# Optimization experiments

Measured on AMD Instinct MI355X. Metric: run time of the kernel, lower is better.

Reference implementation:

```python
import jax, jax.numpy as jnp
import numpy as np

B, C, HD, NL, NP = 2, 256, 8, 4, 4
D = C // HD
SHAPES = np.array([[128, 128], [64, 64], [32, 32], [16, 16]], dtype=np.int64)
LV = int(SHAPES.prod(axis=1).sum())  # 21760
LQ = LV


def _bilinear(v_l, loc, Hl, Wl):
    # v_l: [B, HD, Nl, D]; loc: [B, Q, HD, P, 2] normalized to [0,1]
    # Matches torch grid_sample(bilinear, padding='zeros', align_corners=False)
    Bq, Q, _, P, _ = loc.shape
    x = loc[..., 0] * Wl - 0.5
    y = loc[..., 1] * Hl - 0.5
    x0f = jnp.floor(x)
    y0f = jnp.floor(y)
    lx, ly = x - x0f, y - y0f
    x0 = x0f.astype(jnp.int32)
    y0 = y0f.astype(jnp.int32)

    def corner(xi, yi, w):
        valid = (xi >= 0) & (xi < Wl) & (yi >= 0) & (yi < Hl)
        idx = jnp.clip(yi, 0, Hl - 1) * Wl + jnp.clip(xi, 0, Wl - 1)  # [B,Q,HD,P]
        idx = idx.transpose(0, 2, 1, 3).reshape(Bq, HD, Q * P)
        g = jnp.take_along_axis(v_l, idx[..., None], axis=2).reshape(Bq, HD, Q, P, D)
        wm = jnp.where(valid, w, 0.0).transpose(0, 2, 1, 3)[..., None]  # [B,HD,Q,P,1]
        return g * wm

    return (corner(x0, y0, (1 - lx) * (1 - ly))
            + corner(x0 + 1, y0, lx * (1 - ly))
            + corner(x0, y0 + 1, (1 - lx) * ly)
            + corner(x0 + 1, y0 + 1, lx * ly))


def _msda(query, reference_points, value, shapes, W_off, b_off, W_attn, b_attn, W_val, b_val, W_out, b_out):
    # value projection -> per-head layout [B, HD, Lv, D]
    v = (value @ W_val + b_val).reshape(B, LV, HD, D).transpose(0, 2, 1, 3)
    off = (query @ W_off + b_off).reshape(B, LQ, HD, NL, NP, 2)
    aw = jax.nn.softmax((query @ W_attn + b_attn).reshape(B, LQ, HD, NL * NP), axis=-1)
    aw = aw.reshape(B, LQ, HD, NL, NP)
    norm = jnp.asarray(shapes[:, ::-1].copy(), query.dtype)  # (W_l, H_l) per level
    # sampling locations: [B, Lq, HD, NL, NP, 2]
    loc = reference_points[:, :, None, :, None, :] + off / norm[None, None, None, :, None, :]
    out = jnp.zeros((B, HD, LQ, D), query.dtype)
    start = 0
    for l in range(NL):  # small static loop over feature levels
        Hl, Wl = int(shapes[l, 0]), int(shapes[l, 1])
        samp = _bilinear(v[:, :, start:start + Hl * Wl], loc[:, :, :, l], Hl, Wl)  # [B,HD,Q,P,D]
        out = out + jnp.einsum('bhqpd,bhqp->bhqd', samp, aw[:, :, :, l].transpose(0, 2, 1, 3))
        start += Hl * Wl
    out = out.transpose(0, 2, 1, 3).reshape(B, LQ, C)
    # output projection + residual (identity = query, dropout inactive at eval)
    return out @ W_out + b_out + query


def setup_inputs():
    key = jax.random.key(0)
    ks = jax.random.split(key, 8)
    sc = 1.0 / np.sqrt(C)
    return {
        "query": jax.random.normal(ks[0], (B, LQ, C), jnp.float32),
        "reference_points": jax.random.uniform(ks[1], (B, LQ, NL, 2), dtype=jnp.float32),
        "value": jax.random.normal(ks[2], (B, LV, C), jnp.float32),
        "spatial_shapes": SHAPES,
        "level_start_index": np.concatenate([[0], np.cumsum(SHAPES.prod(axis=1))[:-1]]).astype(np.int64),
        "W_off": jax.random.normal(ks[3], (C, HD * NL * NP * 2), jnp.float32) * 0.01,
        "b_off": jax.random.normal(ks[4], (HD * NL * NP * 2,), jnp.float32) * 0.01,
        "W_attn": jax.random.normal(ks[5], (C, HD * NL * NP), jnp.float32) * 0.02,
        "b_attn": jnp.zeros((HD * NL * NP,), jnp.float32),
        "W_val": jax.random.normal(ks[6], (C, C), jnp.float32) * sc,
        "b_val": jnp.zeros((C,), jnp.float32),
        "W_out": jax.random.normal(ks[7], (C, C), jnp.float32) * sc,
        "b_out": jnp.zeros((C,), jnp.float32),
    }


def reference(query, reference_points, value, spatial_shapes, level_start_index, W_off, b_off, W_attn, b_attn, W_val, b_val, W_out, b_out):
    shapes = np.asarray(spatial_shapes)  # static level geometry
    del level_start_index  # level offsets derived directly from shapes
    return _msda(query, reference_points, value, shapes, W_off, b_off, W_attn, b_attn, W_val, b_val, W_out, b_out)
```

## Files before the change

kernel.cpp:

```cpp
#include <hip/hip_runtime.h>

#define LQN 21760
#define LVN 21760
#define BATCH 2
#define CDIM 256
#define HDN 8
#define DDIM 32
#define PADCELLS 22736

typedef __attribute__((ext_vector_type(8))) short short8;
typedef __attribute__((ext_vector_type(4))) float f32x4;
typedef __attribute__((ext_vector_type(2))) float f32x2;

__device__ __forceinline__ unsigned short f2bf(float f) {
  union { float f; unsigned int u; } v; v.f = f;
  unsigned int r = v.u + 0x7fffu + ((v.u >> 16) & 1u);
  return (unsigned short)(r >> 16);
}
__device__ __forceinline__ float bflo(unsigned int u) {
  union { unsigned int u; float f; } v; v.u = u << 16; return v.f;
}
__device__ __forceinline__ float bfhi(unsigned int u) {
  union { unsigned int u; float f; } v; v.u = u & 0xffff0000u; return v.f;
}

__global__ __launch_bounds__(256) void zero_kernel(uint4* __restrict__ p) {
  const int i = blockIdx.x * 256 + threadIdx.x;
  p[i] = (uint4){0u, 0u, 0u, 0u};
}

__global__ __launch_bounds__(256) void prep_kernel(
    const float* __restrict__ Wval, const float* __restrict__ Woff,
    const float* __restrict__ Wattn, const float* __restrict__ Wout,
    unsigned short* __restrict__ wtval, unsigned short* __restrict__ wtoa,
    unsigned short* __restrict__ wtout) {
  int idx = blockIdx.x * 256 + threadIdx.x;
  int n = idx >> 8, k = idx & 255;
  if (idx < 65536) {
    wtval[idx] = f2bf(Wval[k * 256 + n]);
    wtout[idx] = f2bf(Wout[k * 256 + n]);
  }
  if (idx < 98304) {
    float v = (n < 256) ? Woff[k * 256 + n] : Wattn[k * 128 + (n - 256)];
    wtoa[idx] = f2bf(v);
  }
}

template <int MODE>
__global__ __launch_bounds__(256) void gemm_kernel(
    const float* __restrict__ Af32, const unsigned short* __restrict__ Abf,
    const unsigned short* __restrict__ Wt, const float* __restrict__ bias0,
    const float* __restrict__ bias1, const float* __restrict__ resid,
    unsigned short* __restrict__ out_bf, float* __restrict__ out_f32) {
  constexpr int K = 256;
  constexpr int LDSS = 56;
  __shared__ unsigned short lsA[64 * LDSS];
  __shared__ unsigned short lsB[64 * LDSS];
  const int m0 = blockIdx.x * 64;
  const int n0 = blockIdx.y * 64;
  const int t = threadIdx.x;
  const int w = t >> 6;
  const int l = t & 63;
  const int fr = l & 15;
  const int kk = (l >> 4) * 8;

  f32x4 acc[4];
#pragma unroll
  for (int c = 0; c < 4; ++c) acc[c] = (f32x4){0.f, 0.f, 0.f, 0.f};

  const int srow = t >> 2;
  const int sk = (t & 3) * 8;

  for (int kt = 0; kt < K / 32; ++kt) {
    const int k0 = kt * 32;
    if (MODE == 2) {
      *(uint4*)(lsA + srow * LDSS + sk) =
          *(const uint4*)(Abf + (size_t)(m0 + srow) * K + k0 + sk);
    } else {
      const float* ap = Af32 + (size_t)(m0 + srow) * K + k0 + sk;
      float4 f0 = *(const float4*)(ap);
      float4 f1 = *(const float4*)(ap + 4);
      uint4 pk;
      pk.x = (unsigned)f2bf(f0.x) | ((unsigned)f2bf(f0.y) << 16);
      pk.y = (unsigned)f2bf(f0.z) | ((unsigned)f2bf(f0.w) << 16);
      pk.z = (unsigned)f2bf(f1.x) | ((unsigned)f2bf(f1.y) << 16);
      pk.w = (unsigned)f2bf(f1.z) | ((unsigned)f2bf(f1.w) << 16);
      *(uint4*)(lsA + srow * LDSS + sk) = pk;
    }
    *(uint4*)(lsB + srow * LDSS + sk) =
        *(const uint4*)(Wt + (size_t)(n0 + srow) * K + k0 + sk);
    __syncthreads();
    const short8 a = *(const short8*)(lsA + (w * 16 + fr) * LDSS + kk);
#pragma unroll
    for (int c = 0; c < 4; ++c) {
      const short8 b = *(const short8*)(lsB + (c * 16 + fr) * LDSS + kk);
      acc[c] = __builtin_amdgcn_mfma_f32_16x16x32_bf16(a, b, acc[c], 0, 0, 0);
    }
    __syncthreads();
  }

  const int fq = l >> 4;
#pragma unroll
  for (int c = 0; c < 4; ++c) {
#pragma unroll
    for (int r = 0; r < 4; ++r) {
      const int row = m0 + w * 16 + fq * 4 + r;
      const int col = n0 + c * 16 + fr;
      float v = acc[c][r];
      if (MODE == 0) {
        v += bias0[col];
        const int bb = (row >= LVN) ? 1 : 0;
        const int i = row - bb * LVN;
        const int lvl = (i >= 16384) + (i >= 20480) + (i >= 21504);
        const int stl = (lvl == 0) ? 0 : (lvl == 1) ? 16384 : (lvl == 2) ? 20480 : 21504;
        const int pst = (lvl == 0) ? 0 : (lvl == 1) ? 16900 : (lvl == 2) ? 21256 : 22412;
        const int lw = 7 - lvl;
        const int Wl = 128 >> lvl;
        const int loc = i - stl;
        const int y = loc >> lw;
        const int x = loc & (Wl - 1);
        const int pidx = pst + (y + 1) * (Wl + 2) + (x + 1);
        const int hh = col >> 5, d = col & 31;
        out_bf[(((size_t)(bb * HDN + hh) * PADCELLS + pidx) << 5) + d] = f2bf(v);
      } else if (MODE == 1) {
        const float bias = (col < 256) ? bias0[col] : bias1[col - 256];
        out_bf[(size_t)row * 384 + col] = f2bf(v + bias);
      } else {
        const size_t o = (size_t)row * 256 + col;
        out_f32[o] = v + bias0[col] + resid[o];
      }
    }
  }
}

__global__ __launch_bounds__(256) void sampler_kernel(
    const unsigned short* __restrict__ vbf,
    const unsigned short* __restrict__ offattn,
    const float* __restrict__ refpts,
    unsigned short* __restrict__ msout) {
  const int lid = blockIdx.x;
  const int pair = lid & 7;
  const int k = lid >> 3;
  const int img = pair * 2 + (k & 1);
  const int qchunk = k >> 1;
  const int h = img & 7;
  const int bb = img >> 3;

  const int t = threadIdx.x;
  const int lane = t & 63;
  const int qloc = qchunk * 64 + (t >> 6) * 16 + (lane >> 2);
  const int qi = bb * LQN + qloc;
  const int d0 = (lane & 3) * 8;

  const unsigned short* oa = offattn + (size_t)qi * 384;

  float lg[16];
  {
    const uint4 r0 = *(const uint4*)(oa + 256 + h * 16);
    const uint4 r1 = *(const uint4*)(oa + 256 + h * 16 + 8);
    const unsigned int ww[8] = {r0.x, r0.y, r0.z, r0.w, r1.x, r1.y, r1.z, r1.w};
#pragma unroll
    for (int j = 0; j < 8; ++j) {
      lg[2 * j] = bflo(ww[j]);
      lg[2 * j + 1] = bfhi(ww[j]);
    }
  }
  float mx = lg[0];
#pragma unroll
  for (int j = 1; j < 16; ++j) mx = fmaxf(mx, lg[j]);
  float ssum = 0.f;
#pragma unroll
  for (int j = 0; j < 16; ++j) {
    lg[j] = __expf(lg[j] - mx);
    ssum += lg[j];
  }
  const float inv = 1.f / ssum;
#pragma unroll
  for (int j = 0; j < 16; ++j) lg[j] *= inv;

  const unsigned int headbase =
      (unsigned int)img * (PADCELLS * DDIM) + (unsigned int)d0;

  f32x2 acc0 = (f32x2){0.f, 0.f}, acc1 = (f32x2){0.f, 0.f};
  f32x2 acc2 = (f32x2){0.f, 0.f}, acc3 = (f32x2){0.f, 0.f};

  const float4 refA = *(const float4*)(refpts + (size_t)qi * 8);
  const float4 refB = *(const float4*)(refpts + (size_t)qi * 8 + 4);
  const float rxs[4] = {refA.x, refA.z, refB.x, refB.z};
  const float rys[4] = {refA.y, refA.w, refB.y, refB.w};

#pragma unroll
  for (int lvl = 0; lvl < 4; ++lvl) {
    const int Wl = 128 >> lvl;
    const int W2 = Wl + 2;
    const int pst =
        (lvl == 0) ? 0 : (lvl == 1) ? 16900 : (lvl == 2) ? 21256 : 22412;
    const float fw = (float)Wl;
    const float rx = rxs[lvl], ry = rys[lvl];
    const uint4 ov = *(const uint4*)(oa + h * 32 + lvl * 8);
    const unsigned int op_[4] = {ov.x, ov.y, ov.z, ov.w};
#pragma unroll
    for (int p = 0; p < 4; ++p) {
      const float ox = bflo(op_[p]);
      const float oy = bfhi(op_[p]);
      const float xs = fmaf(rx, fw, ox) - 0.5f;
      const float ys = fmaf(ry, fw, oy) - 0.5f;
      const float x0f = floorf(xs), y0f = floorf(ys);
      const float lx = xs - x0f, ly = ys - y0f;
      const int x0 = (int)x0f, y0 = (int)y0f;
      const float aw = lg[lvl * 4 + p];
      const float wy1 = aw * ly, wy0 = aw - wy1;
      const float w01 = wy0 * lx, w00 = wy0 - w01;
      const float w11 = wy1 * lx, w10 = wy1 - w11;
      const int xb0 = min(max(x0 + 1, 0), Wl + 1);
      const int xb1 = min(max(x0 + 2, 0), Wl + 1);
      const int yb0 = min(max(y0 + 1, 0), Wl + 1);
      const int yb1 = min(max(y0 + 2, 0), Wl + 1);
      const unsigned r0 = (unsigned)(pst + yb0 * W2);
      const unsigned r1 = (unsigned)(pst + yb1 * W2);
      const uint4 v00 = *(const uint4*)(vbf + headbase + ((r0 + xb0) << 5));
      const uint4 v01 = *(const uint4*)(vbf + headbase + ((r0 + xb1) << 5));
      const uint4 v10 = *(const uint4*)(vbf + headbase + ((r1 + xb0) << 5));
      const uint4 v11 = *(const uint4*)(vbf + headbase + ((r1 + xb1) << 5));

#define ACCUM(rv, wgt)                                 \
  {                                                    \
    f32x2 v_;                                          \
    v_.x = bflo(rv.x); v_.y = bfhi(rv.x);              \
    acc0 += v_ * (wgt);                                \
    v_.x = bflo(rv.y); v_.y = bfhi(rv.y);              \
    acc1 += v_ * (wgt);                                \
    v_.x = bflo(rv.z); v_.y = bfhi(rv.z);              \
    acc2 += v_ * (wgt);                                \
    v_.x = bflo(rv.w); v_.y = bfhi(rv.w);              \
    acc3 += v_ * (wgt);                                \
  }

      ACCUM(v00, w00)
      ACCUM(v01, w01)
      ACCUM(v10, w10)
      ACCUM(v11, w11)
#undef ACCUM
    }
  }

  uint4 outv;
  outv.x = (unsigned)f2bf(acc0.x) | ((unsigned)f2bf(acc0.y) << 16);
  outv.y = (unsigned)f2bf(acc1.x) | ((unsigned)f2bf(acc1.y) << 16);
  outv.z = (unsigned)f2bf(acc2.x) | ((unsigned)f2bf(acc2.y) << 16);
  outv.w = (unsigned)f2bf(acc3.x) | ((unsigned)f2bf(acc3.y) << 16);
  *(uint4*)(msout + (size_t)qi * 256 + h * 32 + d0) = outv;
}

extern "C" void kernel_launch(void* const* d_in, const int* in_sizes, int n_in,
                              void* d_out, int out_size, void* d_ws,
                              size_t ws_size, hipStream_t stream) {
  const float* query = (const float*)d_in[0];
  const float* refpts = (const float*)d_in[1];
  const float* value = (const float*)d_in[2];
  const float* W_off = (const float*)d_in[5];
  const float* b_off = (const float*)d_in[6];
  const float* W_attn = (const float*)d_in[7];
  const float* b_attn = (const float*)d_in[8];
  const float* W_val = (const float*)d_in[9];
  const float* b_val = (const float*)d_in[10];
  const float* W_out = (const float*)d_in[11];
  const float* b_out = (const float*)d_in[12];
  float* out = (float*)d_out;

  char* ws = (char*)d_ws;
  unsigned short* wtval = (unsigned short*)(ws);
  unsigned short* wtoa = (unsigned short*)(ws + 131072);
  unsigned short* wtout = (unsigned short*)(ws + 327680);
  unsigned short* vbf = (unsigned short*)(ws + 458752);
  unsigned short* offattn = (unsigned short*)(ws + 23740416);
  unsigned short* msout = (unsigned short*)(ws + 57163776);

  zero_kernel<<<5684, 256, 0, stream>>>((uint4*)vbf);
  prep_kernel<<<384, 256, 0, stream>>>(W_val, W_off, W_attn, W_out, wtval, wtoa,
                                       wtout);
  gemm_kernel<0><<<dim3(680, 4), 256, 0, stream>>>(
      value, nullptr, wtval, b_val, nullptr, nullptr, vbf, nullptr);
  gemm_kernel<1><<<dim3(680, 6), 256, 0, stream>>>(
      query, nullptr, wtoa, b_off, b_attn, nullptr, offattn, nullptr);
  sampler_kernel<<<5440, 256, 0, stream>>>(vbf, offattn, refpts, msout);
  gemm_kernel<2><<<dim3(680, 4), 256, 0, stream>>>(
      nullptr, msout, wtout, b_out, nullptr, query, nullptr, out);
}
```

Before: 186.2 us.

## Enlarge GEMM tiles to 128x128 with 4x4 MFMA fragments per wave

The three projection GEMMs move from 64x64 block tiles, where each wave computes a 16x64 strip, to 128x128 block tiles, where each wave computes a 64x64 sub-tile of 4x4 MFMA fragments. Every A and B fragment loaded from LDS is now reused four times, which raises arithmetic intensity and halves global traffic per output element. The cost is more accumulator registers (64 floats per lane) and a quarter as many blocks (680 to 1020 per GEMM), which may hurt occupancy and load balance on a GPU with many CUs. The LDS row stride also changes from 56 to 40, which alters the bank-conflict pattern.

Measured after the change: 189.7 us. About the same (+1.9%).

```diff
diff --git a/kernel.cpp b/kernel.cpp
--- a/kernel.cpp
+++ b/kernel.cpp
@@ -53,81 +53,106 @@
     const float* __restrict__ bias1, const float* __restrict__ resid,
     unsigned short* __restrict__ out_bf, float* __restrict__ out_f32) {
   constexpr int K = 256;
-  constexpr int LDSS = 56;
-  __shared__ unsigned short lsA[64 * LDSS];
-  __shared__ unsigned short lsB[64 * LDSS];
-  const int m0 = blockIdx.x * 64;
-  const int n0 = blockIdx.y * 64;
+  constexpr int LDSS = 40;
+  __shared__ unsigned short lsA[128 * LDSS];
+  __shared__ unsigned short lsB[128 * LDSS];
+  const int m0 = blockIdx.x * 128;
+  const int n0 = blockIdx.y * 128;
   const int t = threadIdx.x;
   const int w = t >> 6;
   const int l = t & 63;
+  const int wr = (w >> 1) * 64;
+  const int wc = (w & 1) * 64;
   const int fr = l & 15;
   const int kk = (l >> 4) * 8;
 
-  f32x4 acc[4];
-#pragma unroll
-  for (int c = 0; c < 4; ++c) acc[c] = (f32x4){0.f, 0.f, 0.f, 0.f};
-
-  const int srow = t >> 2;
-  const int sk = (t & 3) * 8;
+  f32x4 acc[4][4];
+#pragma unroll
+  for (int mi = 0; mi < 4; ++mi)
+#pragma unroll
+    for (int ci = 0; ci < 4; ++ci) acc[mi][ci] = (f32x4){0.f, 0.f, 0.f, 0.f};
+
+  const int srow = t >> 1;
+  const int sk = (t & 1) * 16;
 
   for (int kt = 0; kt < K / 32; ++kt) {
     const int k0 = kt * 32;
     if (MODE == 2) {
-      *(uint4*)(lsA + srow * LDSS + sk) =
-          *(const uint4*)(Abf + (size_t)(m0 + srow) * K + k0 + sk);
+      const unsigned short* ap = Abf + (size_t)(m0 + srow) * K + k0 + sk;
+      *(uint4*)(lsA + srow * LDSS + sk) = *(const uint4*)(ap);
+      *(uint4*)(lsA + srow * LDSS + sk + 8) = *(const uint4*)(ap + 8);
     } else {
       const float* ap = Af32 + (size_t)(m0 + srow) * K + k0 + sk;
       float4 f0 = *(const float4*)(ap);
       float4 f1 = *(const float4*)(ap + 4);
-      uint4 pk;
-      pk.x = (unsigned)f2bf(f0.x) | ((unsigned)f2bf(f0.y) << 16);
-      pk.y = (unsigned)f2bf(f0.z) | ((unsigned)f2bf(f0.w) << 16);
-      pk.z = (unsigned)f2bf(f1.x) | ((unsigned)f2bf(f1.y) << 16);
-      pk.w = (unsigned)f2bf(f1.z) | ((unsigned)f2bf(f1.w) << 16);
-      *(uint4*)(lsA + srow * LDSS + sk) = pk;
-    }
-    *(uint4*)(lsB + srow * LDSS + sk) =
-        *(const uint4*)(Wt + (size_t)(n0 + srow) * K + k0 + sk);
+      float4 f2 = *(const float4*)(ap + 8);
+      float4 f3 = *(const float4*)(ap + 12);
+      uint4 p0, p1;
+      p0.x = (unsigned)f2bf(f0.x) | ((unsigned)f2bf(f0.y) << 16);
+      p0.y = (unsigned)f2bf(f0.z) | ((unsigned)f2bf(f0.w) << 16);
+      p0.z = (unsigned)f2bf(f1.x) | ((unsigned)f2bf(f1.y) << 16);
+      p0.w = (unsigned)f2bf(f1.z) | ((unsigned)f2bf(f1.w) << 16);
+      p1.x = (unsigned)f2bf(f2.x) | ((unsigned)f2bf(f2.y) << 16);
+      p1.y = (unsigned)f2bf(f2.z) | ((unsigned)f2bf(f2.w) << 16);
+      p1.z = (unsigned)f2bf(f3.x) | ((unsigned)f2bf(f3.y) << 16);
+      p1.w = (unsigned)f2bf(f3.z) | ((unsigned)f2bf(f3.w) << 16);
+      *(uint4*)(lsA + srow * LDSS + sk) = p0;
+      *(uint4*)(lsA + srow * LDSS + sk + 8) = p1;
+    }
+    {
+      const unsigned short* bp = Wt + (size_t)(n0 + srow) * K + k0 + sk;
+      *(uint4*)(lsB + srow * LDSS + sk) = *(const uint4*)(bp);
+      *(uint4*)(lsB + srow * LDSS + sk + 8) = *(const uint4*)(bp + 8);
+    }
     __syncthreads();
-    const short8 a = *(const short8*)(lsA + (w * 16 + fr) * LDSS + kk);
-#pragma unroll
-    for (int c = 0; c < 4; ++c) {
-      const short8 b = *(const short8*)(lsB + (c * 16 + fr) * LDSS + kk);
-      acc[c] = __builtin_amdgcn_mfma_f32_16x16x32_bf16(a, b, acc[c], 0, 0, 0);
-    }
+    short8 af[4], bf[4];
+#pragma unroll
+    for (int mi = 0; mi < 4; ++mi)
+      af[mi] = *(const short8*)(lsA + (wr + mi * 16 + fr) * LDSS + kk);
+#pragma unroll
+    for (int ci = 0; ci < 4; ++ci)
+      bf[ci] = *(const short8*)(lsB + (wc + ci * 16 + fr) * LDSS + kk);
+#pragma unroll
+    for (int mi = 0; mi < 4; ++mi)
+#pragma unroll
+      for (int ci = 0; ci < 4; ++ci)
+        acc[mi][ci] =
+            __builtin_amdgcn_mfma_f32_16x16x32_bf16(af[mi], bf[ci], acc[mi][ci], 0, 0, 0);
     __syncthreads();
   }
 
   const int fq = l >> 4;
 #pragma unroll
-  for (int c = 0; c < 4; ++c) {
-#pragma unroll
-    for (int r = 0; r < 4; ++r) {
-      const int row = m0 + w * 16 + fq * 4 + r;
-      const int col = n0 + c * 16 + fr;
-      float v = acc[c][r];
-      if (MODE == 0) {
-        v += bias0[col];
-        const int bb = (row >= LVN) ? 1 : 0;
-        const int i = row - bb * LVN;
-        const int lvl = (i >= 16384) + (i >= 20480) + (i >= 21504);
-        const int stl = (lvl == 0) ? 0 : (lvl == 1) ? 16384 : (lvl == 2) ? 20480 : 21504;
-        const int pst = (lvl == 0) ? 0 : (lvl == 1) ? 16900 : (lvl == 2) ? 21256 : 22412;
-        const int lw = 7 - lvl;
-        const int Wl = 128 >> lvl;
-        const int loc = i - stl;
-        const int y = loc >> lw;
-        const int x = loc & (Wl - 1);
-        const int pidx = pst + (y + 1) * (Wl + 2) + (x + 1);
-        const int hh = col >> 5, d = col & 31;
-        out_bf[(((size_t)(bb * HDN + hh) * PADCELLS + pidx) << 5) + d] = f2bf(v);
-      } else if (MODE == 1) {
-        const float bias = (col < 256) ? bias0[col] : bias1[col - 256];
-        out_bf[(size_t)row * 384 + col] = f2bf(v + bias);
-      } else {
-        const size_t o = (size_t)row * 256 + col;
-        out_f32[o] = v + bias0[col] + resid[o];
+  for (int mi = 0; mi < 4; ++mi) {
+#pragma unroll
+    for (int ci = 0; ci < 4; ++ci) {
+#pragma unroll
+      for (int r = 0; r < 4; ++r) {
+        const int row = m0 + wr + mi * 16 + fq * 4 + r;
+        const int col = n0 + wc + ci * 16 + fr;
+        float v = acc[mi][ci][r];
+        if (MODE == 0) {
+          v += bias0[col];
+          const int bb = (row >= LVN) ? 1 : 0;
+          const int i = row - bb * LVN;
+          const int lvl = (i >= 16384) + (i >= 20480) + (i >= 21504);
+          const int stl = (lvl == 0) ? 0 : (lvl == 1) ? 16384 : (lvl == 2) ? 20480 : 21504;
+          const int pst = (lvl == 0) ? 0 : (lvl == 1) ? 16900 : (lvl == 2) ? 21256 : 22412;
+          const int lw = 7 - lvl;
+          const int Wl = 128 >> lvl;
+          const int loc = i - stl;
+          const int y = loc >> lw;
+          const int x = loc & (Wl - 1);
+          const int pidx = pst + (y + 1) * (Wl + 2) + (x + 1);
+          const int hh = col >> 5, d = col & 31;
+          out_bf[(((size_t)(bb * HDN + hh) * PADCELLS + pidx) << 5) + d] = f2bf(v);
+        } else if (MODE == 1) {
+          const float bias = (col < 256) ? bias0[col] : bias1[col - 256];
+          out_bf[(size_t)row * 384 + col] = f2bf(v + bias);
+        } else {
+          const size_t o = (size_t)row * 256 + col;
+          out_f32[o] = v + bias0[col] + resid[o];
+        }
       }
     }
   }
@@ -279,11 +304,11 @@
   zero_kernel<<<5684, 256, 0, stream>>>((uint4*)vbf);
   prep_kernel<<<384, 256, 0, stream>>>(W_val, W_off, W_attn, W_out, wtval, wtoa,
                                        wtout);
-  gemm_kernel<0><<<dim3(680, 4), 256, 0, stream>>>(
+  gemm_kernel<0><<<dim3(340, 2), 256, 0, stream>>>(
       value, nullptr, wtval, b_val, nullptr, nullptr, vbf, nullptr);
-  gemm_kernel<1><<<dim3(680, 6), 256, 0, stream>>>(
+  gemm_kernel<1><<<dim3(340, 3), 256, 0, stream>>>(
       query, nullptr, wtoa, b_off, b_attn, nullptr, offattn, nullptr);
   sampler_kernel<<<5440, 256, 0, stream>>>(vbf, offattn, refpts, msout);
-  gemm_kernel<2><<<dim3(680, 4), 256, 0, stream>>>(
+  gemm_kernel<2><<<dim3(340, 2), 256, 0, stream>>>(
       nullptr, msout, wtout, b_out, nullptr, query, nullptr, out);
 }
```
